# Optimization experiments

Measured on AMD Instinct MI355X. Metric: run time of the kernel, lower is better.

## Reference

```python
import jax, jax.numpy as jnp
import numpy as np

B, S, HID = 4, 2048, 512
NH, HD = 8, 64          # num heads, head dim (num_kv_heads == NH, so GQA group = 1)
SW = 250                # sliding window
THETA = 10000.0
SCALING = 1.0 / np.sqrt(HD)
NEG_INF = jnp.finfo(jnp.float32).min


def setup_inputs() -> dict:
    key = jax.random.key(0)
    ks = jax.random.split(key, 5)
    w_std = 1.0 / np.sqrt(HID)
    return {
        "hidden_states": jax.random.normal(ks[0], (B, S, HID), jnp.float32),
        "position_ids": jnp.broadcast_to(jnp.arange(S, dtype=jnp.int64), (B, S)),
        "Wq": jax.random.normal(ks[1], (NH * HD, HID), jnp.float32) * w_std,
        "Wk": jax.random.normal(ks[2], (NH * HD, HID), jnp.float32) * w_std,
        "Wv": jax.random.normal(ks[3], (NH * HD, HID), jnp.float32) * w_std,
        "Wo": jax.random.normal(ks[4], (HID, NH * HD), jnp.float32) * w_std,
    }


def _rotate_half(x):
    x1, x2 = jnp.split(x, 2, axis=-1)
    return jnp.concatenate((-x2, x1), axis=-1)


def reference(hidden_states, position_ids, Wq, Wk, Wv, Wo):
    b, s, _ = hidden_states.shape
    dtype = hidden_states.dtype

    # QKV projections (Linear: x @ W.T, no bias) -> [b, h, s, d]
    q = (hidden_states @ Wq.T).reshape(b, s, NH, HD).transpose(0, 2, 1, 3)
    k = (hidden_states @ Wk.T).reshape(b, s, NH, HD).transpose(0, 2, 1, 3)
    v = (hidden_states @ Wv.T).reshape(b, s, NH, HD).transpose(0, 2, 1, 3)

    # Rotary embedding (MimiRotaryEmbedding), computed in fp32
    inv_freq = 1.0 / (THETA ** (jnp.arange(0, HD, 2, dtype=jnp.float32) / HD))
    freqs = position_ids.astype(jnp.float32)[:, :, None] * inv_freq[None, None, :]  # [b, s, HD/2]
    emb = jnp.concatenate((freqs, freqs), axis=-1)                                   # [b, s, HD]
    cos = jnp.cos(emb).astype(dtype)[:, None, :, :]  # unsqueeze head dim
    sin = jnp.sin(emb).astype(dtype)[:, None, :, :]
    q = q * cos + _rotate_half(q) * sin
    k = k * cos + _rotate_half(k) * sin

    # Sliding-window causal additive mask: keep kv iff q_idx >= kv_idx and q_idx - kv_idx <= SW
    idx = jnp.arange(s)
    keep = (idx[:, None] >= idx[None, :]) & ((idx[:, None] - idx[None, :]) <= SW)
    bias = jnp.where(keep, 0.0, NEG_INF).astype(jnp.float32)  # [s, s]

    # Eager attention: full scores, fp32 softmax (num_key_value_groups == 1)
    scores = jnp.einsum("bhqd,bhkd->bhqk", q, k) * SCALING
    scores = scores.astype(jnp.float32) + bias[None, None, :, :]
    attn = jax.nn.softmax(scores, axis=-1).astype(dtype)
    out = jnp.einsum("bhqk,bhkd->bhqd", attn, v)

    # merge heads and output projection
    out = out.transpose(0, 2, 1, 3).reshape(b, s, NH * HD)
    return out @ Wo.T
```

## Files before the change

kernel.cpp:

```cpp
#include <hip/hip_runtime.h>
#include <hip/hip_bf16.h>
#include <math.h>


#define B_   4
#define S_   2048
#define HID_ 512
#define NH_  8
#define HD_  64
#define SW_  250

typedef __bf16 bf16x8 __attribute__((ext_vector_type(8)));
typedef __bf16 bf16x4 __attribute__((ext_vector_type(4)));
typedef float f32x4 __attribute__((ext_vector_type(4)));
using bf16_t = __hip_bfloat16;
typedef unsigned int u32;

__device__ __forceinline__ void glds16(const bf16_t* g, bf16_t* l) {
    __builtin_amdgcn_global_load_lds(
        (const __attribute__((address_space(1))) u32*)g,
        (__attribute__((address_space(3))) u32*)l, 16, 0, 0);
}

__global__ __launch_bounds__(256) void cvt_all(
    const float* __restrict__ X,  const float* __restrict__ Wq,
    const float* __restrict__ Wk, const float* __restrict__ Wv,
    const float* __restrict__ Wo,
    bf16_t* __restrict__ Xb, bf16_t* __restrict__ Wcat, bf16_t* __restrict__ Wob,
    float2* __restrict__ rope)
{
    const int blk = blockIdx.x;
    if (blk >= 2560) {
        int e0 = ((blk - 2560) * 256 + threadIdx.x) * 4;
#pragma unroll
        for (int j = 0; j < 4; ++j) {
            int e = e0 + j;
            int s = e >> 5, i = e & 31;
            float inv = exp2f(-(float)i * 0.41524101186f);
            float sn, cs;
            sincosf((float)s * inv, &sn, &cs);
            rope[e] = make_float2(cs, sn);
        }
        return;
    }
    const float* s; bf16_t* d; size_t base;
    if (blk < 2048)      { s = X;  d = Xb;            base = (size_t)blk * 2048; }
    else if (blk < 2176) { s = Wq; d = Wcat;          base = (size_t)(blk - 2048) * 2048; }
    else if (blk < 2304) { s = Wk; d = Wcat + 262144; base = (size_t)(blk - 2176) * 2048; }
    else if (blk < 2432) { s = Wv; d = Wcat + 524288; base = (size_t)(blk - 2304) * 2048; }
    else                 { s = Wo; d = Wob;           base = (size_t)(blk - 2432) * 2048; }
    size_t i = base + (size_t)threadIdx.x * 8;
    float4 a = *reinterpret_cast<const float4*>(s + i);
    float4 b = *reinterpret_cast<const float4*>(s + i + 4);
    bf16x8 r;
    r[0] = (__bf16)a.x; r[1] = (__bf16)a.y; r[2] = (__bf16)a.z; r[3] = (__bf16)a.w;
    r[4] = (__bf16)b.x; r[5] = (__bf16)b.y; r[6] = (__bf16)b.z; r[7] = (__bf16)b.w;
    *reinterpret_cast<bf16x8*>(d + i) = r;
}

__global__ __launch_bounds__(256) void qkv_gemm(
    const bf16_t* __restrict__ Xb, const bf16_t* __restrict__ Wcat,
    const float2* __restrict__ rope,
    bf16_t* __restrict__ Q, bf16_t* __restrict__ Kbuf, bf16_t* __restrict__ Vt)
{
    __shared__ __align__(16) bf16_t smem[4 * 64 * 68];
    bf16_t* As = smem;
    bf16_t* Bs = smem + 4096;
    const int tid = threadIdx.x;
    const int wave = tid >> 6, lane = tid & 63;
    const int quad = lane >> 4, l16 = lane & 15;
    const int wm = wave & 1, wn = wave >> 1;
    const int m0 = blockIdx.x * 128, n0 = blockIdx.y * 128;

    f32x4 acc[4][4] = {};
    for (int k0 = 0; k0 < HID_; k0 += 32) {
#pragma unroll
        for (int t = 0; t < 2; ++t) {
            int flat = t * 2048 + tid * 8;
            int row = flat >> 5, col = flat & 31;
            glds16(Xb + (size_t)(m0 + row) * HID_ + k0 + col, As + flat);
            glds16(Wcat + (size_t)(n0 + row) * HID_ + k0 + col, Bs + flat);
        }
        __syncthreads();
        bf16x8 af[4], bfr[4];
#pragma unroll
        for (int i = 0; i < 4; ++i) {
            af[i]  = *reinterpret_cast<const bf16x8*>(&As[(wm * 64 + i * 16 + l16) * 32 + quad * 8]);
            bfr[i] = *reinterpret_cast<const bf16x8*>(&Bs[(wn * 64 + i * 16 + l16) * 32 + quad * 8]);
        }
#pragma unroll
        for (int mi = 0; mi < 4; ++mi)
#pragma unroll
            for (int ni = 0; ni < 4; ++ni)
                acc[mi][ni] = __builtin_amdgcn_mfma_f32_16x16x32_bf16(af[mi], bfr[ni], acc[mi][ni], 0, 0, 0);
        __syncthreads();
    }
    const int seg = n0 >> 9;
    const int npr = n0 & 511;
    const int hh  = (npr + wn * 64) >> 6;
    bf16_t* wt = smem + wave * (64 * 68);
    const int mbase = m0 + wm * 64;
    const int bb = mbase >> 11;
    const int sbase = mbase & (S_ - 1);

    if (seg < 2) {
        const float qs = (seg == 0) ? 0.125f : 1.0f;
#pragma unroll
        for (int mi = 0; mi < 4; ++mi)
#pragma unroll
            for (int r = 0; r < 4; ++r) {
                int lrow = mi * 16 + quad * 4 + r;
                int s = sbase + lrow;
#pragma unroll
                for (int ip = 0; ip < 2; ++ip) {
                    float2 t2 = rope[(size_t)s * 32 + ip * 16 + l16];
                    float x1 = acc[mi][ip][r], x2 = acc[mi][ip + 2][r];
                    wt[lrow * 68 + ip * 16 + l16]      = __float2bfloat16((x1 * t2.x - x2 * t2.y) * qs);
                    wt[lrow * 68 + ip * 16 + l16 + 32] = __float2bfloat16((x2 * t2.x + x1 * t2.y) * qs);
                }
            }
        bf16_t* Y = (seg == 0) ? Q : Kbuf;
#pragma unroll
        for (int it = 0; it < 8; ++it) {
            int e = it * 64 + lane;
            int sr = e >> 3, doff = (e & 7) * 8;
            size_t g = ((size_t)(bb * NH_ + hh) * S_ + sbase + sr) * HD_ + doff;
            *reinterpret_cast<bf16x8*>(Y + g) =
                *reinterpret_cast<const bf16x8*>(wt + sr * 68 + doff);
        }
    } else {
#pragma unroll
        for (int mi = 0; mi < 4; ++mi)
#pragma unroll
            for (int ni = 0; ni < 4; ++ni)
#pragma unroll
                for (int r = 0; r < 4; ++r)
                    wt[(ni * 16 + l16) * 68 + mi * 16 + quad * 4 + r] =
                        __float2bfloat16(acc[mi][ni][r]);
#pragma unroll
        for (int it = 0; it < 8; ++it) {
            int e = it * 64 + lane;
            int d = e >> 3, soff = (e & 7) * 8;
            size_t g = ((size_t)(bb * NH_ + hh) * HD_ + d) * S_ + sbase + soff;
            *reinterpret_cast<bf16x8*>(Vt + g) =
                *reinterpret_cast<const bf16x8*>(wt + d * 68 + soff);
        }
    }
}

__global__ __launch_bounds__(256) void attn_mfma(
    const bf16_t* __restrict__ Q, const bf16_t* __restrict__ K,
    const bf16_t* __restrict__ Vt, bf16_t* __restrict__ A)
{
    __shared__ __align__(16) __bf16 pt[4][16][296];
    __shared__ float sums_l[4][16];
    const int wave = threadIdx.x >> 6, lane = threadIdx.x & 63;
    const int quad = lane >> 4, l16 = lane & 15;
    const int h = blockIdx.y, b = blockIdx.z;
    const int q0 = (blockIdx.x * 4 + wave) * 16;
    const size_t bh  = (size_t)(b * NH_ + h) * S_;
    const size_t bhd = (size_t)(b * NH_ + h) * HD_;

    bf16x8 qf0, qf1;
    {
        const bf16_t* qp = Q + (bh + q0 + l16) * HD_ + quad * 8;
        qf0 = *reinterpret_cast<const bf16x8*>(qp);
        qf1 = *reinterpret_cast<const bf16x8*>(qp + 32);
    }

    const int kstart = (q0 > SW_) ? ((q0 - SW_) & ~31) : 0;
    const int nt = (q0 + 15 - kstart + 32) >> 5;
    const int qq = q0 + l16;

    f32x4 s[9][2];
#pragma unroll
    for (int t = 0; t < 9; ++t) {
        if (t < nt) {
            const int kb = kstart + t * 32;
#pragma unroll
            for (int half = 0; half < 2; ++half) {
                const bf16_t* kp = K + (bh + kb + half * 16 + l16) * HD_ + quad * 8;
                bf16x8 k0 = *reinterpret_cast<const bf16x8*>(kp);
                bf16x8 k1 = *reinterpret_cast<const bf16x8*>(kp + 32);
                f32x4 z = {};
                z = __builtin_amdgcn_mfma_f32_16x16x32_bf16(k0, qf0, z, 0, 0, 0);
                z = __builtin_amdgcn_mfma_f32_16x16x32_bf16(k1, qf1, z, 0, 0, 0);
                const int kbase = kb + half * 16 + quad * 4;
#pragma unroll
                for (int r = 0; r < 4; ++r) {
                    int key = kbase + r;
                    bool keep = (key <= qq) && (qq - key <= SW_);
                    s[t][half][r] = keep ? z[r] : -3.0e38f;
                }
            }
        }
    }

    float mx = -3.0e38f;
#pragma unroll
    for (int t = 0; t < 9; ++t)
        if (t < nt)
#pragma unroll
            for (int half = 0; half < 2; ++half)
#pragma unroll
                for (int r = 0; r < 4; ++r)
                    mx = fmaxf(mx, s[t][half][r]);
    mx = fmaxf(mx, __shfl_xor(mx, 16, 64));
    mx = fmaxf(mx, __shfl_xor(mx, 32, 64));

    float sum = 0.f;
#pragma unroll
    for (int t = 0; t < 9; ++t)
        if (t < nt)
#pragma unroll
            for (int half = 0; half < 2; ++half) {
                bf16x4 pk;
#pragma unroll
                for (int r = 0; r < 4; ++r) {
                    float p = __expf(s[t][half][r] - mx);
                    sum += p;
                    pk[r] = (__bf16)p;
                }
                *reinterpret_cast<bf16x4*>(&pt[wave][l16][t * 32 + half * 16 + quad * 4]) = pk;
            }
    sum += __shfl_xor(sum, 16, 64);
    sum += __shfl_xor(sum, 32, 64);
    if (quad == 0) sums_l[wave][l16] = sum;

    f32x4 o[4] = {};
#pragma unroll
    for (int t = 0; t < 9; ++t) {
        if (t < nt) {
            const int kb = kstart + t * 32;
            bf16x8 pf = *reinterpret_cast<const bf16x8*>(&pt[wave][l16][t * 32 + quad * 8]);
#pragma unroll
            for (int nf = 0; nf < 4; ++nf) {
                const bf16_t* vp = Vt + (bhd + nf * 16 + l16) * S_ + kb + quad * 8;
                bf16x8 vf = *reinterpret_cast<const bf16x8*>(vp);
                o[nf] = __builtin_amdgcn_mfma_f32_16x16x32_bf16(pf, vf, o[nf], 0, 0, 0);
            }
        }
    }

    float inv_l[4];
#pragma unroll
    for (int r = 0; r < 4; ++r) inv_l[r] = 1.0f / sums_l[wave][quad * 4 + r];
#pragma unroll
    for (int nf = 0; nf < 4; ++nf)
#pragma unroll
        for (int r = 0; r < 4; ++r) {
            int qr = q0 + quad * 4 + r;
            A[((size_t)(b * S_ + qr)) * HID_ + h * HD_ + nf * 16 + l16] =
                __float2bfloat16(o[nf][r] * inv_l[r]);
        }
}

__global__ __launch_bounds__(256) void out_proj(
    const bf16_t* __restrict__ Ain, const bf16_t* __restrict__ Wob,
    float* __restrict__ out)
{
    __shared__ __align__(16) bf16_t As[128 * 32];
    __shared__ __align__(16) bf16_t Bs[64 * 32];
    const int tid = threadIdx.x;
    const int wave = tid >> 6, lane = tid & 63;
    const int quad = lane >> 4, l16 = lane & 15;
    const int m0 = blockIdx.x * 128, n0 = blockIdx.y * 64;

    f32x4 acc[2][4] = {};
    for (int k0 = 0; k0 < HID_; k0 += 32) {
#pragma unroll
        for (int t = 0; t < 2; ++t) {
            int flat = t * 2048 + tid * 8;
            int row = flat >> 5, col = flat & 31;
            glds16(Ain + (size_t)(m0 + row) * HID_ + k0 + col, As + flat);
        }
        {
            int flat = tid * 8;
            int row = flat >> 5, col = flat & 31;
            glds16(Wob + (size_t)(n0 + row) * HID_ + k0 + col, Bs + flat);
        }
        __syncthreads();
        bf16x8 af[2], bfr[4];
#pragma unroll
        for (int i = 0; i < 2; ++i)
            af[i] = *reinterpret_cast<const bf16x8*>(&As[(wave * 32 + i * 16 + l16) * 32 + quad * 8]);
#pragma unroll
        for (int i = 0; i < 4; ++i)
            bfr[i] = *reinterpret_cast<const bf16x8*>(&Bs[(i * 16 + l16) * 32 + quad * 8]);
#pragma unroll
        for (int mi = 0; mi < 2; ++mi)
#pragma unroll
            for (int ni = 0; ni < 4; ++ni)
                acc[mi][ni] = __builtin_amdgcn_mfma_f32_16x16x32_bf16(af[mi], bfr[ni], acc[mi][ni], 0, 0, 0);
        __syncthreads();
    }
#pragma unroll
    for (int mi = 0; mi < 2; ++mi)
#pragma unroll
        for (int ni = 0; ni < 4; ++ni)
#pragma unroll
            for (int r = 0; r < 4; ++r) {
                int m = m0 + wave * 32 + mi * 16 + quad * 4 + r;
                int n = n0 + ni * 16 + l16;
                out[(size_t)m * HID_ + n] = acc[mi][ni][r];
            }
}

extern "C" void kernel_launch(void* const* d_in, const int* in_sizes, int n_in,
                              void* d_out, int out_size, void* d_ws, size_t ws_size,
                              hipStream_t stream)
{
    const float* X  = (const float*)d_in[0];
    const float* Wq = (const float*)d_in[2];
    const float* Wk = (const float*)d_in[3];
    const float* Wv = (const float*)d_in[4];
    const float* Wo = (const float*)d_in[5];

    char* ws = (char*)d_ws;
    const size_t elems = (size_t)B_ * NH_ * S_ * HD_;
    const size_t wsz   = (size_t)HID_ * HID_;
    bf16_t* Q    = (bf16_t*)ws;
    bf16_t* K    = Q + elems;
    bf16_t* Vt   = K + elems;
    bf16_t* Xb   = Vt + elems;
    bf16_t* A    = Xb;
    bf16_t* Wcat = Xb + elems;
    bf16_t* Wob  = Wcat + 3 * wsz;
    float2* rope = (float2*)(Wob + wsz);

    cvt_all<<<2624, 256, 0, stream>>>(X, Wq, Wk, Wv, Wo, Xb, Wcat, Wob, rope);
    qkv_gemm<<<dim3(64, 12), 256, 0, stream>>>(Xb, Wcat, rope, Q, K, Vt);
    attn_mfma<<<dim3(32, 8, 4), 256, 0, stream>>>(Q, K, Vt, A);
    out_proj<<<dim3(64, 8), 256, 0, stream>>>(A, Wob, (float*)d_out);
}
```

Measured before the change: 146.9 us.

## Fuse four kernels into one persistent kernel with grid-wide barriers

Replaces the four separate launches (convert, QKV GEMM, attention, output projection) with a single persistent kernel of 512 blocks that loops over each stage's work items and separates stages with atomic-counter grid barriers. The aim is to remove per-launch overhead and inter-kernel gaps. In exchange it adds a memset launch, spin-wait barriers that assume every block is co-resident, and a separate A buffer because Xb can no longer be aliased. Per-stage parallelism is now fixed at 512 blocks, which may leave some stages underloaded or unevenly balanced.

New measurement: 415.1 us. 182% more time.

```diff
diff --git a/kernel.cpp b/kernel.cpp
--- a/kernel.cpp
+++ b/kernel.cpp
@@ -9,6 +9,7 @@
 #define NH_  8
 #define HD_  64
 #define SW_  250
+#define GRID_ 512
 
 typedef __bf16 bf16x8 __attribute__((ext_vector_type(8)));
 typedef __bf16 bf16x4 __attribute__((ext_vector_type(4)));
@@ -22,288 +23,291 @@
         (__attribute__((address_space(3))) u32*)l, 16, 0, 0);
 }
 
-__global__ __launch_bounds__(256) void cvt_all(
-    const float* __restrict__ X,  const float* __restrict__ Wq,
-    const float* __restrict__ Wk, const float* __restrict__ Wv,
-    const float* __restrict__ Wo,
-    bf16_t* __restrict__ Xb, bf16_t* __restrict__ Wcat, bf16_t* __restrict__ Wob,
-    float2* __restrict__ rope)
+__device__ __forceinline__ void grid_barrier(int* cnt) {
+    __syncthreads();
+    if (threadIdx.x == 0) {
+        __threadfence();
+        __hip_atomic_fetch_add(cnt, 1, __ATOMIC_ACQ_REL, __HIP_MEMORY_SCOPE_AGENT);
+        while (__hip_atomic_load(cnt, __ATOMIC_ACQUIRE, __HIP_MEMORY_SCOPE_AGENT) < GRID_)
+            __builtin_amdgcn_s_sleep(8);
+        __threadfence();
+    }
+    __syncthreads();
+}
+
+__global__ __launch_bounds__(256, 2) void fused(
+    const float* X,  const float* Wq, const float* Wk, const float* Wv,
+    const float* Wo,
+    bf16_t* Xb, bf16_t* Wcat, bf16_t* Wob, float2* rope,
+    bf16_t* Q, bf16_t* K, bf16_t* Vt, bf16_t* A, float* out, int* bar)
 {
-    const int blk = blockIdx.x;
-    if (blk >= 2560) {
-        int e0 = ((blk - 2560) * 256 + threadIdx.x) * 4;
-#pragma unroll
-        for (int j = 0; j < 4; ++j) {
-            int e = e0 + j;
-            int s = e >> 5, i = e & 31;
-            float inv = exp2f(-(float)i * 0.41524101186f);
-            float sn, cs;
-            sincosf((float)s * inv, &sn, &cs);
-            rope[e] = make_float2(cs, sn);
-        }
-        return;
-    }
-    const float* s; bf16_t* d; size_t base;
-    if (blk < 2048)      { s = X;  d = Xb;            base = (size_t)blk * 2048; }
-    else if (blk < 2176) { s = Wq; d = Wcat;          base = (size_t)(blk - 2048) * 2048; }
-    else if (blk < 2304) { s = Wk; d = Wcat + 262144; base = (size_t)(blk - 2176) * 2048; }
-    else if (blk < 2432) { s = Wv; d = Wcat + 524288; base = (size_t)(blk - 2304) * 2048; }
-    else                 { s = Wo; d = Wob;           base = (size_t)(blk - 2432) * 2048; }
-    size_t i = base + (size_t)threadIdx.x * 8;
-    float4 a = *reinterpret_cast<const float4*>(s + i);
-    float4 b = *reinterpret_cast<const float4*>(s + i + 4);
-    bf16x8 r;
-    r[0] = (__bf16)a.x; r[1] = (__bf16)a.y; r[2] = (__bf16)a.z; r[3] = (__bf16)a.w;
-    r[4] = (__bf16)b.x; r[5] = (__bf16)b.y; r[6] = (__bf16)b.z; r[7] = (__bf16)b.w;
-    *reinterpret_cast<bf16x8*>(d + i) = r;
-}
-
-__global__ __launch_bounds__(256) void qkv_gemm(
-    const bf16_t* __restrict__ Xb, const bf16_t* __restrict__ Wcat,
-    const float2* __restrict__ rope,
-    bf16_t* __restrict__ Q, bf16_t* __restrict__ Kbuf, bf16_t* __restrict__ Vt)
-{
-    __shared__ __align__(16) bf16_t smem[4 * 64 * 68];
-    bf16_t* As = smem;
-    bf16_t* Bs = smem + 4096;
+    __shared__ __align__(16) char smem_raw[39168];
     const int tid = threadIdx.x;
     const int wave = tid >> 6, lane = tid & 63;
     const int quad = lane >> 4, l16 = lane & 15;
-    const int wm = wave & 1, wn = wave >> 1;
-    const int m0 = blockIdx.x * 128, n0 = blockIdx.y * 128;
-
-    f32x4 acc[4][4] = {};
-    for (int k0 = 0; k0 < HID_; k0 += 32) {
-#pragma unroll
-        for (int t = 0; t < 2; ++t) {
-            int flat = t * 2048 + tid * 8;
-            int row = flat >> 5, col = flat & 31;
-            glds16(Xb + (size_t)(m0 + row) * HID_ + k0 + col, As + flat);
-            glds16(Wcat + (size_t)(n0 + row) * HID_ + k0 + col, Bs + flat);
+
+    for (int blk = blockIdx.x; blk < 2624; blk += GRID_) {
+        if (blk >= 2560) {
+            int e0 = ((blk - 2560) * 256 + tid) * 4;
+#pragma unroll
+            for (int j = 0; j < 4; ++j) {
+                int e = e0 + j;
+                int s = e >> 5, i = e & 31;
+                float inv = exp2f(-(float)i * 0.41524101186f);
+                float sn, cs;
+                sincosf((float)s * inv, &sn, &cs);
+                rope[e] = make_float2(cs, sn);
+            }
+            continue;
         }
-        __syncthreads();
-        bf16x8 af[4], bfr[4];
-#pragma unroll
-        for (int i = 0; i < 4; ++i) {
-            af[i]  = *reinterpret_cast<const bf16x8*>(&As[(wm * 64 + i * 16 + l16) * 32 + quad * 8]);
-            bfr[i] = *reinterpret_cast<const bf16x8*>(&Bs[(wn * 64 + i * 16 + l16) * 32 + quad * 8]);
+        const float* s; bf16_t* d; size_t base;
+        if (blk < 2048)      { s = X;  d = Xb;            base = (size_t)blk * 2048; }
+        else if (blk < 2176) { s = Wq; d = Wcat;          base = (size_t)(blk - 2048) * 2048; }
+        else if (blk < 2304) { s = Wk; d = Wcat + 262144; base = (size_t)(blk - 2176) * 2048; }
+        else if (blk < 2432) { s = Wv; d = Wcat + 524288; base = (size_t)(blk - 2304) * 2048; }
+        else                 { s = Wo; d = Wob;           base = (size_t)(blk - 2432) * 2048; }
+        size_t i = base + (size_t)tid * 8;
+        float4 a = *reinterpret_cast<const float4*>(s + i);
+        float4 b = *reinterpret_cast<const float4*>(s + i + 4);
+        bf16x8 r;
+        r[0] = (__bf16)a.x; r[1] = (__bf16)a.y; r[2] = (__bf16)a.z; r[3] = (__bf16)a.w;
+        r[4] = (__bf16)b.x; r[5] = (__bf16)b.y; r[6] = (__bf16)b.z; r[7] = (__bf16)b.w;
+        *reinterpret_cast<bf16x8*>(d + i) = r;
+    }
+    grid_barrier(bar + 0);
+
+    {
+        bf16_t* As = (bf16_t*)smem_raw;
+        bf16_t* Bs = As + 4096;
+        const int wm = wave & 1, wn = wave >> 1;
+        for (int t = blockIdx.x; t < 768; t += GRID_) {
+            __syncthreads();
+            const int m0 = (t & 63) * 128, n0 = (t >> 6) * 128;
+            f32x4 acc[4][4] = {};
+            for (int k0 = 0; k0 < HID_; k0 += 32) {
+#pragma unroll
+                for (int tt = 0; tt < 2; ++tt) {
+                    int flat = tt * 2048 + tid * 8;
+                    int row = flat >> 5, col = flat & 31;
+                    glds16(Xb + (size_t)(m0 + row) * HID_ + k0 + col, As + flat);
+                    glds16(Wcat + (size_t)(n0 + row) * HID_ + k0 + col, Bs + flat);
+                }
+                __syncthreads();
+                bf16x8 af[4], bfr[4];
+#pragma unroll
+                for (int i = 0; i < 4; ++i) {
+                    af[i]  = *reinterpret_cast<const bf16x8*>(&As[(wm * 64 + i * 16 + l16) * 32 + quad * 8]);
+                    bfr[i] = *reinterpret_cast<const bf16x8*>(&Bs[(wn * 64 + i * 16 + l16) * 32 + quad * 8]);
+                }
+#pragma unroll
+                for (int mi = 0; mi < 4; ++mi)
+#pragma unroll
+                    for (int ni = 0; ni < 4; ++ni)
+                        acc[mi][ni] = __builtin_amdgcn_mfma_f32_16x16x32_bf16(af[mi], bfr[ni], acc[mi][ni], 0, 0, 0);
+                __syncthreads();
+            }
+            const int seg = n0 >> 9;
+            const int hh  = ((n0 & 511) + wn * 64) >> 6;
+            bf16_t* wt = (bf16_t*)smem_raw + wave * 4352;
+            const int mbase = m0 + wm * 64;
+            const int bb = mbase >> 11;
+            const int sbase = mbase & (S_ - 1);
+
+            if (seg < 2) {
+                const float qs = (seg == 0) ? 0.125f : 1.0f;
+#pragma unroll
+                for (int mi = 0; mi < 4; ++mi)
+#pragma unroll
+                    for (int r = 0; r < 4; ++r) {
+                        int lrow = mi * 16 + quad * 4 + r;
+                        int s = sbase + lrow;
+#pragma unroll
+                        for (int ip = 0; ip < 2; ++ip) {
+                            float2 t2 = rope[(size_t)s * 32 + ip * 16 + l16];
+                            float x1 = acc[mi][ip][r], x2 = acc[mi][ip + 2][r];
+                            wt[lrow * 68 + ip * 16 + l16]      = __float2bfloat16((x1 * t2.x - x2 * t2.y) * qs);
+                            wt[lrow * 68 + ip * 16 + l16 + 32] = __float2bfloat16((x2 * t2.x + x1 * t2.y) * qs);
+                        }
+                    }
+                bf16_t* Y = (seg == 0) ? Q : K;
+#pragma unroll
+                for (int it = 0; it < 8; ++it) {
+                    int e = it * 64 + lane;
+                    int sr = e >> 3, doff = (e & 7) * 8;
+                    size_t g = ((size_t)(bb * NH_ + hh) * S_ + sbase + sr) * HD_ + doff;
+                    *reinterpret_cast<bf16x8*>(Y + g) =
+                        *reinterpret_cast<const bf16x8*>(wt + sr * 68 + doff);
+                }
+            } else {
+#pragma unroll
+                for (int mi = 0; mi < 4; ++mi)
+#pragma unroll
+                    for (int ni = 0; ni < 4; ++ni)
+#pragma unroll
+                        for (int r = 0; r < 4; ++r)
+                            wt[(ni * 16 + l16) * 68 + mi * 16 + quad * 4 + r] =
+                                __float2bfloat16(acc[mi][ni][r]);
+#pragma unroll
+                for (int it = 0; it < 8; ++it) {
+                    int e = it * 64 + lane;
+                    int d = e >> 3, soff = (e & 7) * 8;
+                    size_t g = ((size_t)(bb * NH_ + hh) * HD_ + d) * S_ + sbase + soff;
+                    *reinterpret_cast<bf16x8*>(Vt + g) =
+                        *reinterpret_cast<const bf16x8*>(wt + d * 68 + soff);
+                }
+            }
         }
-#pragma unroll
-        for (int mi = 0; mi < 4; ++mi)
+    }
+    grid_barrier(bar + 1);
+
+    {
+        __bf16* pt = (__bf16*)smem_raw;
+        float* sums_l = (float*)(smem_raw + 37888);
+        for (int v = blockIdx.x; v < 1024; v += GRID_) {
+            const int h = (v >> 5) & 7, b = v >> 8;
+            const int q0 = ((v & 31) * 4 + wave) * 16;
+            const size_t bh  = (size_t)(b * NH_ + h) * S_;
+            const size_t bhd = (size_t)(b * NH_ + h) * HD_;
+
+            bf16x8 qf0, qf1;
+            {
+                const bf16_t* qp = Q + (bh + q0 + l16) * HD_ + quad * 8;
+                qf0 = *reinterpret_cast<const bf16x8*>(qp);
+                qf1 = *reinterpret_cast<const bf16x8*>(qp + 32);
+            }
+            const int kstart = (q0 > SW_) ? ((q0 - SW_) & ~31) : 0;
+            const int nt = (q0 + 15 - kstart + 32) >> 5;
+            const int qq = q0 + l16;
+
+            f32x4 s[9][2];
+#pragma unroll
+            for (int t = 0; t < 9; ++t) {
+                if (t < nt) {
+                    const int kb = kstart + t * 32;
+#pragma unroll
+                    for (int half = 0; half < 2; ++half) {
+                        const bf16_t* kp = K + (bh + kb + half * 16 + l16) * HD_ + quad * 8;
+                        bf16x8 k0 = *reinterpret_cast<const bf16x8*>(kp);
+                        bf16x8 k1 = *reinterpret_cast<const bf16x8*>(kp + 32);
+                        f32x4 z = {};
+                        z = __builtin_amdgcn_mfma_f32_16x16x32_bf16(k0, qf0, z, 0, 0, 0);
+                        z = __builtin_amdgcn_mfma_f32_16x16x32_bf16(k1, qf1, z, 0, 0, 0);
+                        const int kbase = kb + half * 16 + quad * 4;
+#pragma unroll
+                        for (int r = 0; r < 4; ++r) {
+                            int key = kbase + r;
+                            bool keep = (key <= qq) && (qq - key <= SW_);
+                            s[t][half][r] = keep ? z[r] : -3.0e38f;
+                        }
+                    }
+                }
+            }
+            float mx = -3.0e38f;
+#pragma unroll
+            for (int t = 0; t < 9; ++t)
+                if (t < nt)
+#pragma unroll
+                    for (int half = 0; half < 2; ++half)
+#pragma unroll
+                        for (int r = 0; r < 4; ++r)
+                            mx = fmaxf(mx, s[t][half][r]);
+            mx = fmaxf(mx, __shfl_xor(mx, 16, 64));
+            mx = fmaxf(mx, __shfl_xor(mx, 32, 64));
+
+            float sum = 0.f;
+#pragma unroll
+            for (int t = 0; t < 9; ++t)
+                if (t < nt)
+#pragma unroll
+                    for (int half = 0; half < 2; ++half) {
+                        bf16x4 pk;
+#pragma unroll
+                        for (int r = 0; r < 4; ++r) {
+                            float p = __expf(s[t][half][r] - mx);
+                            sum += p;
+                            pk[r] = (__bf16)p;
+                        }
+                        *reinterpret_cast<bf16x4*>(
+                            &pt[(wave * 16 + l16) * 296 + t * 32 + half * 16 + quad * 4]) = pk;
+                    }
+            sum += __shfl_xor(sum, 16, 64);
+            sum += __shfl_xor(sum, 32, 64);
+            if (quad == 0) sums_l[wave * 16 + l16] = sum;
+
+            f32x4 o[4] = {};
+#pragma unroll
+            for (int t = 0; t < 9; ++t) {
+                if (t < nt) {
+                    const int kb = kstart + t * 32;
+                    bf16x8 pf = *reinterpret_cast<const bf16x8*>(
+                        &pt[(wave * 16 + l16) * 296 + t * 32 + quad * 8]);
+#pragma unroll
+                    for (int nf = 0; nf < 4; ++nf) {
+                        const bf16_t* vp = Vt + (bhd + nf * 16 + l16) * S_ + kb + quad * 8;
+                        bf16x8 vf = *reinterpret_cast<const bf16x8*>(vp);
+                        o[nf] = __builtin_amdgcn_mfma_f32_16x16x32_bf16(pf, vf, o[nf], 0, 0, 0);
+                    }
+                }
+            }
+            float inv_l[4];
+#pragma unroll
+            for (int r = 0; r < 4; ++r) inv_l[r] = 1.0f / sums_l[wave * 16 + quad * 4 + r];
+#pragma unroll
+            for (int nf = 0; nf < 4; ++nf)
+#pragma unroll
+                for (int r = 0; r < 4; ++r) {
+                    int qr = q0 + quad * 4 + r;
+                    A[((size_t)(b * S_ + qr)) * HID_ + h * HD_ + nf * 16 + l16] =
+                        __float2bfloat16(o[nf][r] * inv_l[r]);
+                }
+        }
+    }
+    grid_barrier(bar + 2);
+
+    {
+        bf16_t* As = (bf16_t*)smem_raw;
+        bf16_t* Bs = As + 4096;
+        const int v = blockIdx.x;
+        const int m0 = (v & 63) * 128, n0 = (v >> 6) * 64;
+        f32x4 acc[2][4] = {};
+        for (int k0 = 0; k0 < HID_; k0 += 32) {
+#pragma unroll
+            for (int tt = 0; tt < 2; ++tt) {
+                int flat = tt * 2048 + tid * 8;
+                int row = flat >> 5, col = flat & 31;
+                glds16(A + (size_t)(m0 + row) * HID_ + k0 + col, As + flat);
+            }
+            {
+                int flat = tid * 8;
+                int row = flat >> 5, col = flat & 31;
+                glds16(Wob + (size_t)(n0 + row) * HID_ + k0 + col, Bs + flat);
+            }
+            __syncthreads();
+            bf16x8 af[2], bfr[4];
+#pragma unroll
+            for (int i = 0; i < 2; ++i)
+                af[i] = *reinterpret_cast<const bf16x8*>(&As[(wave * 32 + i * 16 + l16) * 32 + quad * 8]);
+#pragma unroll
+            for (int i = 0; i < 4; ++i)
+                bfr[i] = *reinterpret_cast<const bf16x8*>(&Bs[(i * 16 + l16) * 32 + quad * 8]);
+#pragma unroll
+            for (int mi = 0; mi < 2; ++mi)
+#pragma unroll
+                for (int ni = 0; ni < 4; ++ni)
+                    acc[mi][ni] = __builtin_amdgcn_mfma_f32_16x16x32_bf16(af[mi], bfr[ni], acc[mi][ni], 0, 0, 0);
+            __syncthreads();
+        }
+#pragma unroll
+        for (int mi = 0; mi < 2; ++mi)
 #pragma unroll
             for (int ni = 0; ni < 4; ++ni)
-                acc[mi][ni] = __builtin_amdgcn_mfma_f32_16x16x32_bf16(af[mi], bfr[ni], acc[mi][ni], 0, 0, 0);
-        __syncthreads();
-    }
-    const int seg = n0 >> 9;
-    const int npr = n0 & 511;
-    const int hh  = (npr + wn * 64) >> 6;
-    bf16_t* wt = smem + wave * (64 * 68);
-    const int mbase = m0 + wm * 64;
-    const int bb = mbase >> 11;
-    const int sbase = mbase & (S_ - 1);
-
-    if (seg < 2) {
-        const float qs = (seg == 0) ? 0.125f : 1.0f;
-#pragma unroll
-        for (int mi = 0; mi < 4; ++mi)
-#pragma unroll
-            for (int r = 0; r < 4; ++r) {
-                int lrow = mi * 16 + quad * 4 + r;
-                int s = sbase + lrow;
-#pragma unroll
-                for (int ip = 0; ip < 2; ++ip) {
-                    float2 t2 = rope[(size_t)s * 32 + ip * 16 + l16];
-                    float x1 = acc[mi][ip][r], x2 = acc[mi][ip + 2][r];
-                    wt[lrow * 68 + ip * 16 + l16]      = __float2bfloat16((x1 * t2.x - x2 * t2.y) * qs);
-                    wt[lrow * 68 + ip * 16 + l16 + 32] = __float2bfloat16((x2 * t2.x + x1 * t2.y) * qs);
-                }
-            }
-        bf16_t* Y = (seg == 0) ? Q : Kbuf;
-#pragma unroll
-        for (int it = 0; it < 8; ++it) {
-            int e = it * 64 + lane;
-            int sr = e >> 3, doff = (e & 7) * 8;
-            size_t g = ((size_t)(bb * NH_ + hh) * S_ + sbase + sr) * HD_ + doff;
-            *reinterpret_cast<bf16x8*>(Y + g) =
-                *reinterpret_cast<const bf16x8*>(wt + sr * 68 + doff);
-        }
-    } else {
-#pragma unroll
-        for (int mi = 0; mi < 4; ++mi)
-#pragma unroll
-            for (int ni = 0; ni < 4; ++ni)
-#pragma unroll
-                for (int r = 0; r < 4; ++r)
-                    wt[(ni * 16 + l16) * 68 + mi * 16 + quad * 4 + r] =
-                        __float2bfloat16(acc[mi][ni][r]);
-#pragma unroll
-        for (int it = 0; it < 8; ++it) {
-            int e = it * 64 + lane;
-            int d = e >> 3, soff = (e & 7) * 8;
-            size_t g = ((size_t)(bb * NH_ + hh) * HD_ + d) * S_ + sbase + soff;
-            *reinterpret_cast<bf16x8*>(Vt + g) =
-                *reinterpret_cast<const bf16x8*>(wt + d * 68 + soff);
-        }
-    }
-}
-
-__global__ __launch_bounds__(256) void attn_mfma(
-    const bf16_t* __restrict__ Q, const bf16_t* __restrict__ K,
-    const bf16_t* __restrict__ Vt, bf16_t* __restrict__ A)
-{
-    __shared__ __align__(16) __bf16 pt[4][16][296];
-    __shared__ float sums_l[4][16];
-    const int wave = threadIdx.x >> 6, lane = threadIdx.x & 63;
-    const int quad = lane >> 4, l16 = lane & 15;
-    const int h = blockIdx.y, b = blockIdx.z;
-    const int q0 = (blockIdx.x * 4 + wave) * 16;
-    const size_t bh  = (size_t)(b * NH_ + h) * S_;
-    const size_t bhd = (size_t)(b * NH_ + h) * HD_;
-
-    bf16x8 qf0, qf1;
-    {
-        const bf16_t* qp = Q + (bh + q0 + l16) * HD_ + quad * 8;
-        qf0 = *reinterpret_cast<const bf16x8*>(qp);
-        qf1 = *reinterpret_cast<const bf16x8*>(qp + 32);
-    }
-
-    const int kstart = (q0 > SW_) ? ((q0 - SW_) & ~31) : 0;
-    const int nt = (q0 + 15 - kstart + 32) >> 5;
-    const int qq = q0 + l16;
-
-    f32x4 s[9][2];
-#pragma unroll
-    for (int t = 0; t < 9; ++t) {
-        if (t < nt) {
-            const int kb = kstart + t * 32;
-#pragma unroll
-            for (int half = 0; half < 2; ++half) {
-                const bf16_t* kp = K + (bh + kb + half * 16 + l16) * HD_ + quad * 8;
-                bf16x8 k0 = *reinterpret_cast<const bf16x8*>(kp);
-                bf16x8 k1 = *reinterpret_cast<const bf16x8*>(kp + 32);
-                f32x4 z = {};
-                z = __builtin_amdgcn_mfma_f32_16x16x32_bf16(k0, qf0, z, 0, 0, 0);
-                z = __builtin_amdgcn_mfma_f32_16x16x32_bf16(k1, qf1, z, 0, 0, 0);
-                const int kbase = kb + half * 16 + quad * 4;
 #pragma unroll
                 for (int r = 0; r < 4; ++r) {
-                    int key = kbase + r;
-                    bool keep = (key <= qq) && (qq - key <= SW_);
-                    s[t][half][r] = keep ? z[r] : -3.0e38f;
-                }
-            }
-        }
-    }
-
-    float mx = -3.0e38f;
-#pragma unroll
-    for (int t = 0; t < 9; ++t)
-        if (t < nt)
-#pragma unroll
-            for (int half = 0; half < 2; ++half)
-#pragma unroll
-                for (int r = 0; r < 4; ++r)
-                    mx = fmaxf(mx, s[t][half][r]);
-    mx = fmaxf(mx, __shfl_xor(mx, 16, 64));
-    mx = fmaxf(mx, __shfl_xor(mx, 32, 64));
-
-    float sum = 0.f;
-#pragma unroll
-    for (int t = 0; t < 9; ++t)
-        if (t < nt)
-#pragma unroll
-            for (int half = 0; half < 2; ++half) {
-                bf16x4 pk;
-#pragma unroll
-                for (int r = 0; r < 4; ++r) {
-                    float p = __expf(s[t][half][r] - mx);
-                    sum += p;
-                    pk[r] = (__bf16)p;
-                }
-                *reinterpret_cast<bf16x4*>(&pt[wave][l16][t * 32 + half * 16 + quad * 4]) = pk;
-            }
-    sum += __shfl_xor(sum, 16, 64);
-    sum += __shfl_xor(sum, 32, 64);
-    if (quad == 0) sums_l[wave][l16] = sum;
-
-    f32x4 o[4] = {};
-#pragma unroll
-    for (int t = 0; t < 9; ++t) {
-        if (t < nt) {
-            const int kb = kstart + t * 32;
-            bf16x8 pf = *reinterpret_cast<const bf16x8*>(&pt[wave][l16][t * 32 + quad * 8]);
-#pragma unroll
-            for (int nf = 0; nf < 4; ++nf) {
-                const bf16_t* vp = Vt + (bhd + nf * 16 + l16) * S_ + kb + quad * 8;
-                bf16x8 vf = *reinterpret_cast<const bf16x8*>(vp);
-                o[nf] = __builtin_amdgcn_mfma_f32_16x16x32_bf16(pf, vf, o[nf], 0, 0, 0);
-            }
-        }
-    }
-
-    float inv_l[4];
-#pragma unroll
-    for (int r = 0; r < 4; ++r) inv_l[r] = 1.0f / sums_l[wave][quad * 4 + r];
-#pragma unroll
-    for (int nf = 0; nf < 4; ++nf)
-#pragma unroll
-        for (int r = 0; r < 4; ++r) {
-            int qr = q0 + quad * 4 + r;
-            A[((size_t)(b * S_ + qr)) * HID_ + h * HD_ + nf * 16 + l16] =
-                __float2bfloat16(o[nf][r] * inv_l[r]);
-        }
-}
-
-__global__ __launch_bounds__(256) void out_proj(
-    const bf16_t* __restrict__ Ain, const bf16_t* __restrict__ Wob,
-    float* __restrict__ out)
-{
-    __shared__ __align__(16) bf16_t As[128 * 32];
-    __shared__ __align__(16) bf16_t Bs[64 * 32];
-    const int tid = threadIdx.x;
-    const int wave = tid >> 6, lane = tid & 63;
-    const int quad = lane >> 4, l16 = lane & 15;
-    const int m0 = blockIdx.x * 128, n0 = blockIdx.y * 64;
-
-    f32x4 acc[2][4] = {};
-    for (int k0 = 0; k0 < HID_; k0 += 32) {
-#pragma unroll
-        for (int t = 0; t < 2; ++t) {
-            int flat = t * 2048 + tid * 8;
-            int row = flat >> 5, col = flat & 31;
-            glds16(Ain + (size_t)(m0 + row) * HID_ + k0 + col, As + flat);
-        }
-        {
-            int flat = tid * 8;
-            int row = flat >> 5, col = flat & 31;
-            glds16(Wob + (size_t)(n0 + row) * HID_ + k0 + col, Bs + flat);
-        }
-        __syncthreads();
-        bf16x8 af[2], bfr[4];
-#pragma unroll
-        for (int i = 0; i < 2; ++i)
-            af[i] = *reinterpret_cast<const bf16x8*>(&As[(wave * 32 + i * 16 + l16) * 32 + quad * 8]);
-#pragma unroll
-        for (int i = 0; i < 4; ++i)
-            bfr[i] = *reinterpret_cast<const bf16x8*>(&Bs[(i * 16 + l16) * 32 + quad * 8]);
-#pragma unroll
-        for (int mi = 0; mi < 2; ++mi)
-#pragma unroll
-            for (int ni = 0; ni < 4; ++ni)
-                acc[mi][ni] = __builtin_amdgcn_mfma_f32_16x16x32_bf16(af[mi], bfr[ni], acc[mi][ni], 0, 0, 0);
-        __syncthreads();
-    }
-#pragma unroll
-    for (int mi = 0; mi < 2; ++mi)
-#pragma unroll
-        for (int ni = 0; ni < 4; ++ni)
-#pragma unroll
-            for (int r = 0; r < 4; ++r) {
-                int m = m0 + wave * 32 + mi * 16 + quad * 4 + r;
-                int n = n0 + ni * 16 + l16;
-                out[(size_t)m * HID_ + n] = acc[mi][ni][r];
-            }
+                    int m = m0 + wave * 32 + mi * 16 + quad * 4 + r;
+                    int n = n0 + ni * 16 + l16;
+                    out[(size_t)m * HID_ + n] = acc[mi][ni][r];
+                }
+    }
 }
 
 extern "C" void kernel_launch(void* const* d_in, const int* in_sizes, int n_in,
@@ -315,6 +319,7 @@
     const float* Wk = (const float*)d_in[3];
     const float* Wv = (const float*)d_in[4];
     const float* Wo = (const float*)d_in[5];
+    float* outp = (float*)d_out;
 
     char* ws = (char*)d_ws;
     const size_t elems = (size_t)B_ * NH_ * S_ * HD_;
@@ -323,13 +328,14 @@
     bf16_t* K    = Q + elems;
     bf16_t* Vt   = K + elems;
     bf16_t* Xb   = Vt + elems;
-    bf16_t* A    = Xb;
-    bf16_t* Wcat = Xb + elems;
+    bf16_t* A    = Xb + elems;
+    bf16_t* Wcat = A + elems;
     bf16_t* Wob  = Wcat + 3 * wsz;
     float2* rope = (float2*)(Wob + wsz);
-
-    cvt_all<<<2624, 256, 0, stream>>>(X, Wq, Wk, Wv, Wo, Xb, Wcat, Wob, rope);
-    qkv_gemm<<<dim3(64, 12), 256, 0, stream>>>(Xb, Wcat, rope, Q, K, Vt);
-    attn_mfma<<<dim3(32, 8, 4), 256, 0, stream>>>(Q, K, Vt, A);
-    out_proj<<<dim3(64, 8), 256, 0, stream>>>(A, Wob, (float*)d_out);
+    int*    bar  = (int*)(rope + 65536);
+
+    hipMemsetAsync(bar, 0, 3 * sizeof(int), stream);
+    fused<<<GRID_, 256, 0, stream>>>(X, Wq, Wk, Wv, Wo,
+                                     Xb, Wcat, Wob, rope,
+                                     Q, K, Vt, A, outp, bar);
 }
```

## Fuse fp32-to-bf16 conversion and RoPE table into GEMM kernels, drop cvt_all

Applied to the files above, without the earlier changes.

Removes the separate conversion kernel. The QKV and output-projection GEMMs now load fp32 X and weights straight into LDS and convert fragments to bf16 in registers. RoPE cos/sin values are computed inline with fast __sincosf instead of being read from a precomputed table. This saves one launch and a full round trip of the converted activations and weights through memory, but doubles the LDS traffic per tile, adds conversion ALU work in the GEMM inner loop, and uses lower-precision fast sincos.

After: 305.6 us. +108.0%, slower.

```diff
diff --git a/kernel.cpp b/kernel.cpp
--- a/kernel.cpp
+++ b/kernel.cpp
@@ -16,77 +16,55 @@
 using bf16_t = __hip_bfloat16;
 typedef unsigned int u32;
 
-__device__ __forceinline__ void glds16(const bf16_t* g, bf16_t* l) {
+__device__ __forceinline__ void glds16(const void* g, void* l) {
     __builtin_amdgcn_global_load_lds(
         (const __attribute__((address_space(1))) u32*)g,
         (__attribute__((address_space(3))) u32*)l, 16, 0, 0);
 }
 
-__global__ __launch_bounds__(256) void cvt_all(
-    const float* __restrict__ X,  const float* __restrict__ Wq,
-    const float* __restrict__ Wk, const float* __restrict__ Wv,
-    const float* __restrict__ Wo,
-    bf16_t* __restrict__ Xb, bf16_t* __restrict__ Wcat, bf16_t* __restrict__ Wob,
-    float2* __restrict__ rope)
-{
-    const int blk = blockIdx.x;
-    if (blk >= 2560) {
-        int e0 = ((blk - 2560) * 256 + threadIdx.x) * 4;
-#pragma unroll
-        for (int j = 0; j < 4; ++j) {
-            int e = e0 + j;
-            int s = e >> 5, i = e & 31;
-            float inv = exp2f(-(float)i * 0.41524101186f);
-            float sn, cs;
-            sincosf((float)s * inv, &sn, &cs);
-            rope[e] = make_float2(cs, sn);
-        }
-        return;
-    }
-    const float* s; bf16_t* d; size_t base;
-    if (blk < 2048)      { s = X;  d = Xb;            base = (size_t)blk * 2048; }
-    else if (blk < 2176) { s = Wq; d = Wcat;          base = (size_t)(blk - 2048) * 2048; }
-    else if (blk < 2304) { s = Wk; d = Wcat + 262144; base = (size_t)(blk - 2176) * 2048; }
-    else if (blk < 2432) { s = Wv; d = Wcat + 524288; base = (size_t)(blk - 2304) * 2048; }
-    else                 { s = Wo; d = Wob;           base = (size_t)(blk - 2432) * 2048; }
-    size_t i = base + (size_t)threadIdx.x * 8;
-    float4 a = *reinterpret_cast<const float4*>(s + i);
-    float4 b = *reinterpret_cast<const float4*>(s + i + 4);
+__device__ __forceinline__ bf16x8 frag_cvt(const float* p) {
+    float4 a = *reinterpret_cast<const float4*>(p);
+    float4 b = *reinterpret_cast<const float4*>(p + 4);
     bf16x8 r;
     r[0] = (__bf16)a.x; r[1] = (__bf16)a.y; r[2] = (__bf16)a.z; r[3] = (__bf16)a.w;
     r[4] = (__bf16)b.x; r[5] = (__bf16)b.y; r[6] = (__bf16)b.z; r[7] = (__bf16)b.w;
-    *reinterpret_cast<bf16x8*>(d + i) = r;
+    return r;
 }
 
 __global__ __launch_bounds__(256) void qkv_gemm(
-    const bf16_t* __restrict__ Xb, const bf16_t* __restrict__ Wcat,
-    const float2* __restrict__ rope,
+    const float* __restrict__ X,
+    const float* __restrict__ Wq, const float* __restrict__ Wk,
+    const float* __restrict__ Wv,
     bf16_t* __restrict__ Q, bf16_t* __restrict__ Kbuf, bf16_t* __restrict__ Vt)
 {
-    __shared__ __align__(16) bf16_t smem[4 * 64 * 68];
-    bf16_t* As = smem;
-    bf16_t* Bs = smem + 4096;
+    __shared__ __align__(16) char smem_raw[34816];
+    float* As = (float*)smem_raw;
+    float* Bs = As + 4096;
     const int tid = threadIdx.x;
     const int wave = tid >> 6, lane = tid & 63;
     const int quad = lane >> 4, l16 = lane & 15;
     const int wm = wave & 1, wn = wave >> 1;
     const int m0 = blockIdx.x * 128, n0 = blockIdx.y * 128;
 
+    const int seg = n0 >> 9;
+    const float* W = (seg == 0) ? Wq : (seg == 1) ? Wk : Wv;
+    const int nrow0 = n0 & 511;
+
     f32x4 acc[4][4] = {};
     for (int k0 = 0; k0 < HID_; k0 += 32) {
 #pragma unroll
-        for (int t = 0; t < 2; ++t) {
-            int flat = t * 2048 + tid * 8;
+        for (int rr = 0; rr < 4; ++rr) {
+            int flat = rr * 1024 + tid * 4;
             int row = flat >> 5, col = flat & 31;
-            glds16(Xb + (size_t)(m0 + row) * HID_ + k0 + col, As + flat);
-            glds16(Wcat + (size_t)(n0 + row) * HID_ + k0 + col, Bs + flat);
+            glds16(X + (size_t)(m0 + row) * HID_ + k0 + col, As + flat);
+            glds16(W + (size_t)(nrow0 + row) * HID_ + k0 + col, Bs + flat);
         }
         __syncthreads();
         bf16x8 af[4], bfr[4];
 #pragma unroll
         for (int i = 0; i < 4; ++i) {
-            af[i]  = *reinterpret_cast<const bf16x8*>(&As[(wm * 64 + i * 16 + l16) * 32 + quad * 8]);
-            bfr[i] = *reinterpret_cast<const bf16x8*>(&Bs[(wn * 64 + i * 16 + l16) * 32 + quad * 8]);
+            af[i]  = frag_cvt(&As[(wm * 64 + i * 16 + l16) * 32 + quad * 8]);
+            bfr[i] = frag_cvt(&Bs[(wn * 64 + i * 16 + l16) * 32 + quad * 8]);
         }
 #pragma unroll
         for (int mi = 0; mi < 4; ++mi)
@@ -95,28 +73,31 @@
                 acc[mi][ni] = __builtin_amdgcn_mfma_f32_16x16x32_bf16(af[mi], bfr[ni], acc[mi][ni], 0, 0, 0);
         __syncthreads();
     }
-    const int seg = n0 >> 9;
-    const int npr = n0 & 511;
-    const int hh  = (npr + wn * 64) >> 6;
-    bf16_t* wt = smem + wave * (64 * 68);
+
+    const int hh = ((n0 & 511) + wn * 64) >> 6;
+    bf16_t* wt = (bf16_t*)smem_raw + wave * 4352;
     const int mbase = m0 + wm * 64;
     const int bb = mbase >> 11;
     const int sbase = mbase & (S_ - 1);
 
     if (seg < 2) {
         const float qs = (seg == 0) ? 0.125f : 1.0f;
+        const float c = 0.41524101186f;
+        float inv0 = exp2f(-(float)l16 * c);
+        float inv1 = exp2f(-(float)(l16 + 16) * c);
 #pragma unroll
         for (int mi = 0; mi < 4; ++mi)
 #pragma unroll
             for (int r = 0; r < 4; ++r) {
                 int lrow = mi * 16 + quad * 4 + r;
-                int s = sbase + lrow;
+                float sf = (float)(sbase + lrow);
 #pragma unroll
                 for (int ip = 0; ip < 2; ++ip) {
-                    float2 t2 = rope[(size_t)s * 32 + ip * 16 + l16];
+                    float sn, cs_;
+                    __sincosf(sf * (ip ? inv1 : inv0), &sn, &cs_);
                     float x1 = acc[mi][ip][r], x2 = acc[mi][ip + 2][r];
-                    wt[lrow * 68 + ip * 16 + l16]      = __float2bfloat16((x1 * t2.x - x2 * t2.y) * qs);
-                    wt[lrow * 68 + ip * 16 + l16 + 32] = __float2bfloat16((x2 * t2.x + x1 * t2.y) * qs);
+                    wt[lrow * 68 + ip * 16 + l16]      = __float2bfloat16((x1 * cs_ - x2 * sn) * qs);
+                    wt[lrow * 68 + ip * 16 + l16 + 32] = __float2bfloat16((x2 * cs_ + x1 * sn) * qs);
                 }
             }
         bf16_t* Y = (seg == 0) ? Q : Kbuf;
@@ -167,7 +148,6 @@
         qf0 = *reinterpret_cast<const bf16x8*>(qp);
         qf1 = *reinterpret_cast<const bf16x8*>(qp + 32);
     }
-
     const int kstart = (q0 > SW_) ? ((q0 - SW_) & ~31) : 0;
     const int nt = (q0 + 15 - kstart + 32) >> 5;
     const int qq = q0 + l16;
@@ -195,7 +175,6 @@
             }
         }
     }
-
     float mx = -3.0e38f;
 #pragma unroll
     for (int t = 0; t < 9; ++t)
@@ -241,7 +220,6 @@
             }
         }
     }
-
     float inv_l[4];
 #pragma unroll
     for (int r = 0; r < 4; ++r) inv_l[r] = 1.0f / sums_l[wave][quad * 4 + r];
@@ -256,11 +234,11 @@
 }
 
 __global__ __launch_bounds__(256) void out_proj(
-    const bf16_t* __restrict__ Ain, const bf16_t* __restrict__ Wob,
+    const bf16_t* __restrict__ Ain, const float* __restrict__ Wo,
     float* __restrict__ out)
 {
     __shared__ __align__(16) bf16_t As[128 * 32];
-    __shared__ __align__(16) bf16_t Bs[64 * 32];
+    __shared__ __align__(16) float  Bs[64 * 32];
     const int tid = threadIdx.x;
     const int wave = tid >> 6, lane = tid & 63;
     const int quad = lane >> 4, l16 = lane & 15;
@@ -269,15 +247,16 @@
     f32x4 acc[2][4] = {};
     for (int k0 = 0; k0 < HID_; k0 += 32) {
 #pragma unroll
-        for (int t = 0; t < 2; ++t) {
-            int flat = t * 2048 + tid * 8;
+        for (int tt = 0; tt < 2; ++tt) {
+            int flat = tt * 2048 + tid * 8;
             int row = flat >> 5, col = flat & 31;
             glds16(Ain + (size_t)(m0 + row) * HID_ + k0 + col, As + flat);
         }
-        {
-            int flat = tid * 8;
+#pragma unroll
+        for (int rr = 0; rr < 2; ++rr) {
+            int flat = rr * 1024 + tid * 4;
             int row = flat >> 5, col = flat & 31;
-            glds16(Wob + (size_t)(n0 + row) * HID_ + k0 + col, Bs + flat);
+            glds16(Wo + (size_t)(n0 + row) * HID_ + k0 + col, Bs + flat);
         }
         __syncthreads();
         bf16x8 af[2], bfr[4];
@@ -286,7 +265,7 @@
             af[i] = *reinterpret_cast<const bf16x8*>(&As[(wave * 32 + i * 16 + l16) * 32 + quad * 8]);
 #pragma unroll
         for (int i = 0; i < 4; ++i)
-            bfr[i] = *reinterpret_cast<const bf16x8*>(&Bs[(i * 16 + l16) * 32 + quad * 8]);
+            bfr[i] = frag_cvt(&Bs[(i * 16 + l16) * 32 + quad * 8]);
 #pragma unroll
         for (int mi = 0; mi < 2; ++mi)
 #pragma unroll
@@ -318,18 +297,12 @@
 
     char* ws = (char*)d_ws;
     const size_t elems = (size_t)B_ * NH_ * S_ * HD_;
-    const size_t wsz   = (size_t)HID_ * HID_;
-    bf16_t* Q    = (bf16_t*)ws;
-    bf16_t* K    = Q + elems;
-    bf16_t* Vt   = K + elems;
-    bf16_t* Xb   = Vt + elems;
-    bf16_t* A    = Xb;
-    bf16_t* Wcat = Xb + elems;
-    bf16_t* Wob  = Wcat + 3 * wsz;
-    float2* rope = (float2*)(Wob + wsz);
-
-    cvt_all<<<2624, 256, 0, stream>>>(X, Wq, Wk, Wv, Wo, Xb, Wcat, Wob, rope);
-    qkv_gemm<<<dim3(64, 12), 256, 0, stream>>>(Xb, Wcat, rope, Q, K, Vt);
+    bf16_t* Q  = (bf16_t*)ws;
+    bf16_t* K  = Q + elems;
+    bf16_t* Vt = K + elems;
+    bf16_t* A  = Vt + elems;
+
+    qkv_gemm<<<dim3(64, 12), 256, 0, stream>>>(X, Wq, Wk, Wv, Q, K, Vt);
     attn_mfma<<<dim3(32, 8, 4), 256, 0, stream>>>(Q, K, Vt, A);
-    out_proj<<<dim3(64, 8), 256, 0, stream>>>(A, Wob, (float*)d_out);
-}
+    out_proj<<<dim3(64, 8), 256, 0, stream>>>(A, Wo, (float*)d_out);
+}
```

## Swizzle GEMM LDS tiles and compute RoPE inline in QKV epilogue

Applied to the files above, without the earlier changes.

Applies an XOR swizzle to the 16-byte chunks loaded into LDS in both the QKV and output-projection GEMMs, so the per-quad fragment reads hit different banks. It also drops the precomputed rope table from the conversion kernel and computes sin/cos directly in the QKV epilogue with fast __sincosf. This removes a global table write and read plus 64 conversion blocks. The trade-off is lower-accuracy trig at large positions, which could shift results slightly.

New measurement: 145.4 us, median of 2. About the same (-1.1%).

```diff
diff --git a/kernel.cpp b/kernel.cpp
--- a/kernel.cpp
+++ b/kernel.cpp
@@ -16,7 +16,7 @@
 using bf16_t = __hip_bfloat16;
 typedef unsigned int u32;
 
-__device__ __forceinline__ void glds16(const bf16_t* g, bf16_t* l) {
+__device__ __forceinline__ void glds16(const void* g, void* l) {
     __builtin_amdgcn_global_load_lds(
         (const __attribute__((address_space(1))) u32*)g,
         (__attribute__((address_space(3))) u32*)l, 16, 0, 0);
@@ -26,23 +26,9 @@
     const float* __restrict__ X,  const float* __restrict__ Wq,
     const float* __restrict__ Wk, const float* __restrict__ Wv,
     const float* __restrict__ Wo,
-    bf16_t* __restrict__ Xb, bf16_t* __restrict__ Wcat, bf16_t* __restrict__ Wob,
-    float2* __restrict__ rope)
+    bf16_t* __restrict__ Xb, bf16_t* __restrict__ Wcat, bf16_t* __restrict__ Wob)
 {
     const int blk = blockIdx.x;
-    if (blk >= 2560) {
-        int e0 = ((blk - 2560) * 256 + threadIdx.x) * 4;
-#pragma unroll
-        for (int j = 0; j < 4; ++j) {
-            int e = e0 + j;
-            int s = e >> 5, i = e & 31;
-            float inv = exp2f(-(float)i * 0.41524101186f);
-            float sn, cs;
-            sincosf((float)s * inv, &sn, &cs);
-            rope[e] = make_float2(cs, sn);
-        }
-        return;
-    }
     const float* s; bf16_t* d; size_t base;
     if (blk < 2048)      { s = X;  d = Xb;            base = (size_t)blk * 2048; }
     else if (blk < 2176) { s = Wq; d = Wcat;          base = (size_t)(blk - 2048) * 2048; }
@@ -60,12 +46,11 @@
 
 __global__ __launch_bounds__(256) void qkv_gemm(
     const bf16_t* __restrict__ Xb, const bf16_t* __restrict__ Wcat,
-    const float2* __restrict__ rope,
     bf16_t* __restrict__ Q, bf16_t* __restrict__ Kbuf, bf16_t* __restrict__ Vt)
 {
-    __shared__ __align__(16) bf16_t smem[4 * 64 * 68];
-    bf16_t* As = smem;
-    bf16_t* Bs = smem + 4096;
+    __shared__ __align__(16) char smem_raw[34816];
+    bf16_t* As = (bf16_t*)smem_raw;
+    bf16_t* Bs = As + 4096;
     const int tid = threadIdx.x;
     const int wave = tid >> 6, lane = tid & 63;
     const int quad = lane >> 4, l16 = lane & 15;
@@ -75,18 +60,23 @@
     f32x4 acc[4][4] = {};
     for (int k0 = 0; k0 < HID_; k0 += 32) {
 #pragma unroll
-        for (int t = 0; t < 2; ++t) {
-            int flat = t * 2048 + tid * 8;
-            int row = flat >> 5, col = flat & 31;
-            glds16(Xb + (size_t)(m0 + row) * HID_ + k0 + col, As + flat);
-            glds16(Wcat + (size_t)(n0 + row) * HID_ + k0 + col, Bs + flat);
+        for (int rr = 0; rr < 2; ++rr) {
+            int slot = rr * 256 + tid;
+            int row = slot >> 2;
+            int l = (slot & 3) ^ ((row >> 1) & 3);
+            glds16(Xb + (size_t)(m0 + row) * HID_ + k0 + l * 8, As + slot * 8);
+            glds16(Wcat + (size_t)(n0 + row) * HID_ + k0 + l * 8, Bs + slot * 8);
         }
         __syncthreads();
         bf16x8 af[4], bfr[4];
 #pragma unroll
         for (int i = 0; i < 4; ++i) {
-            af[i]  = *reinterpret_cast<const bf16x8*>(&As[(wm * 64 + i * 16 + l16) * 32 + quad * 8]);
-            bfr[i] = *reinterpret_cast<const bf16x8*>(&Bs[(wn * 64 + i * 16 + l16) * 32 + quad * 8]);
+            int ra = wm * 64 + i * 16 + l16;
+            int rb = wn * 64 + i * 16 + l16;
+            int pa = quad ^ ((ra >> 1) & 3);
+            int pb = quad ^ ((rb >> 1) & 3);
+            af[i]  = *reinterpret_cast<const bf16x8*>(&As[ra * 32 + pa * 8]);
+            bfr[i] = *reinterpret_cast<const bf16x8*>(&Bs[rb * 32 + pb * 8]);
         }
 #pragma unroll
         for (int mi = 0; mi < 4; ++mi)
@@ -95,28 +85,32 @@
                 acc[mi][ni] = __builtin_amdgcn_mfma_f32_16x16x32_bf16(af[mi], bfr[ni], acc[mi][ni], 0, 0, 0);
         __syncthreads();
     }
+
     const int seg = n0 >> 9;
-    const int npr = n0 & 511;
-    const int hh  = (npr + wn * 64) >> 6;
-    bf16_t* wt = smem + wave * (64 * 68);
+    const int hh = ((n0 & 511) + wn * 64) >> 6;
+    bf16_t* wt = (bf16_t*)smem_raw + wave * 4352;
     const int mbase = m0 + wm * 64;
     const int bb = mbase >> 11;
     const int sbase = mbase & (S_ - 1);
 
     if (seg < 2) {
         const float qs = (seg == 0) ? 0.125f : 1.0f;
+        const float c = 0.41524101186f;
+        float inv0 = exp2f(-(float)l16 * c);
+        float inv1 = exp2f(-(float)(l16 + 16) * c);
 #pragma unroll
         for (int mi = 0; mi < 4; ++mi)
 #pragma unroll
             for (int r = 0; r < 4; ++r) {
                 int lrow = mi * 16 + quad * 4 + r;
-                int s = sbase + lrow;
+                float sf = (float)(sbase + lrow);
 #pragma unroll
                 for (int ip = 0; ip < 2; ++ip) {
-                    float2 t2 = rope[(size_t)s * 32 + ip * 16 + l16];
+                    float sn, cs_;
+                    __sincosf(sf * (ip ? inv1 : inv0), &sn, &cs_);
                     float x1 = acc[mi][ip][r], x2 = acc[mi][ip + 2][r];
-                    wt[lrow * 68 + ip * 16 + l16]      = __float2bfloat16((x1 * t2.x - x2 * t2.y) * qs);
-                    wt[lrow * 68 + ip * 16 + l16 + 32] = __float2bfloat16((x2 * t2.x + x1 * t2.y) * qs);
+                    wt[lrow * 68 + ip * 16 + l16]      = __float2bfloat16((x1 * cs_ - x2 * sn) * qs);
+                    wt[lrow * 68 + ip * 16 + l16 + 32] = __float2bfloat16((x2 * cs_ + x1 * sn) * qs);
                 }
             }
         bf16_t* Y = (seg == 0) ? Q : Kbuf;
@@ -167,7 +161,6 @@
         qf0 = *reinterpret_cast<const bf16x8*>(qp);
         qf1 = *reinterpret_cast<const bf16x8*>(qp + 32);
     }
-
     const int kstart = (q0 > SW_) ? ((q0 - SW_) & ~31) : 0;
     const int nt = (q0 + 15 - kstart + 32) >> 5;
     const int qq = q0 + l16;
@@ -195,7 +188,6 @@
             }
         }
     }
-
     float mx = -3.0e38f;
 #pragma unroll
     for (int t = 0; t < 9; ++t)
@@ -241,7 +233,6 @@
             }
         }
     }
-
     float inv_l[4];
 #pragma unroll
     for (int r = 0; r < 4; ++r) inv_l[r] = 1.0f / sums_l[wave][quad * 4 + r];
@@ -269,24 +260,32 @@
     f32x4 acc[2][4] = {};
     for (int k0 = 0; k0 < HID_; k0 += 32) {
 #pragma unroll
-        for (int t = 0; t < 2; ++t) {
-            int flat = t * 2048 + tid * 8;
-            int row = flat >> 5, col = flat & 31;
-            glds16(Ain + (size_t)(m0 + row) * HID_ + k0 + col, As + flat);
+        for (int rr = 0; rr < 2; ++rr) {
+            int slot = rr * 256 + tid;
+            int row = slot >> 2;
+            int l = (slot & 3) ^ ((row >> 1) & 3);
+            glds16(Ain + (size_t)(m0 + row) * HID_ + k0 + l * 8, As + slot * 8);
         }
         {
-            int flat = tid * 8;
-            int row = flat >> 5, col = flat & 31;
-            glds16(Wob + (size_t)(n0 + row) * HID_ + k0 + col, Bs + flat);
+            int slot = tid;
+            int row = slot >> 2;
+            int l = (slot & 3) ^ ((row >> 1) & 3);
+            glds16(Wob + (size_t)(n0 + row) * HID_ + k0 + l * 8, Bs + slot * 8);
         }
         __syncthreads();
         bf16x8 af[2], bfr[4];
 #pragma unroll
-        for (int i = 0; i < 2; ++i)
-            af[i] = *reinterpret_cast<const bf16x8*>(&As[(wave * 32 + i * 16 + l16) * 32 + quad * 8]);
-#pragma unroll
-        for (int i = 0; i < 4; ++i)
-            bfr[i] = *reinterpret_cast<const bf16x8*>(&Bs[(i * 16 + l16) * 32 + quad * 8]);
+        for (int i = 0; i < 2; ++i) {
+            int ra = wave * 32 + i * 16 + l16;
+            int pa = quad ^ ((ra >> 1) & 3);
+            af[i] = *reinterpret_cast<const bf16x8*>(&As[ra * 32 + pa * 8]);
+        }
+#pragma unroll
+        for (int i = 0; i < 4; ++i) {
+            int rb = i * 16 + l16;
+            int pb = quad ^ ((rb >> 1) & 3);
+            bfr[i] = *reinterpret_cast<const bf16x8*>(&Bs[rb * 32 + pb * 8]);
+        }
 #pragma unroll
         for (int mi = 0; mi < 2; ++mi)
 #pragma unroll
@@ -326,10 +325,9 @@
     bf16_t* A    = Xb;
     bf16_t* Wcat = Xb + elems;
     bf16_t* Wob  = Wcat + 3 * wsz;
-    float2* rope = (float2*)(Wob + wsz);
-
-    cvt_all<<<2624, 256, 0, stream>>>(X, Wq, Wk, Wv, Wo, Xb, Wcat, Wob, rope);
-    qkv_gemm<<<dim3(64, 12), 256, 0, stream>>>(Xb, Wcat, rope, Q, K, Vt);
+
+    cvt_all<<<2560, 256, 0, stream>>>(X, Wq, Wk, Wv, Wo, Xb, Wcat, Wob);
+    qkv_gemm<<<dim3(64, 12), 256, 0, stream>>>(Xb, Wcat, Q, K, Vt);
     attn_mfma<<<dim3(32, 8, 4), 256, 0, stream>>>(Q, K, Vt, A);
     out_proj<<<dim3(64, 8), 256, 0, stream>>>(A, Wob, (float*)d_out);
 }
```
